# Performance work log

Measured on AMD Instinct MI355X. Metric: run time of the kernel, lower is better.

The kernel has to match this reference:

```python
import jax, jax.numpy as jnp
import numpy as np

NHID = 768
H = 128        # LSTM hidden per direction
NHEADS = 6
NDIR = 12      # 6 heads x 2 directions; first 6 = forward, last 6 = backward
DFF = 4 * NHID
CAT = 2 * H * NHEADS  # 1536


def setup_inputs() -> dict:
    key = jax.random.key(0)
    ks = jax.random.split(key, 12)
    s = 0.05
    return {
        "embeddings": jax.random.normal(ks[0], (16, 512, NHID), jnp.float32),
        # stacked LSTM params; gate order i,f,g,o as in PyTorch
        "W_ih": jax.random.normal(ks[1], (NDIR, 4 * H, NHID), jnp.float32) * s,
        "W_hh": jax.random.normal(ks[2], (NDIR, 4 * H, H), jnp.float32) * s,
        "b_ih": jax.random.normal(ks[3], (NDIR, 4 * H), jnp.float32) * s,
        "b_hh": jax.random.normal(ks[4], (NDIR, 4 * H), jnp.float32) * s,
        "W_int": jax.random.normal(ks[5], (DFF, CAT), jnp.float32) * s,
        "b_int": jax.random.normal(ks[6], (DFF,), jnp.float32) * s,
        "W_out": jax.random.normal(ks[7], (NHID, DFF), jnp.float32) * s,
        "b_out": jax.random.normal(ks[8], (NHID,), jnp.float32) * s,
        "gamma": jnp.ones((NHID,), jnp.float32),
        "beta": jnp.zeros((NHID,), jnp.float32),
    }


def _multi_bilstm(x, W_ih, W_hh, b_ih, b_hh):
    # x: [B,S,D] -> concat of 6 bidirectional LSTM outputs [B,S,1536]
    B, S, _ = x.shape
    # input projections for all 12 directions at once: [12,B,S,4H]
    xp = jnp.einsum('bsd,kgd->kbsg', x, W_ih) + (b_ih + b_hh)[:, None, None, :]
    # reverse time for the 6 backward directions
    xp = jnp.concatenate([xp[:NHEADS], xp[NHEADS:, :, ::-1]], axis=0)
    xs = jnp.moveaxis(xp, 2, 0)  # [S,12,B,4H]

    def step(carry, z_x):
        h, c = carry  # each [12,B,H]
        z = z_x + jnp.einsum('kbh,kgh->kbg', h, W_hh)
        i, f, g, o = jnp.split(z, 4, axis=-1)
        c = jax.nn.sigmoid(f) * c + jax.nn.sigmoid(i) * jnp.tanh(g)
        h = jax.nn.sigmoid(o) * jnp.tanh(c)
        return (h, c), h

    init = (jnp.zeros((NDIR, B, H), x.dtype), jnp.zeros((NDIR, B, H), x.dtype))
    _, ys = jax.lax.scan(step, init, xs)        # [S,12,B,H]
    ys = jnp.moveaxis(ys, 0, 2)                 # [12,B,S,H]
    ys = jnp.concatenate([ys[:NHEADS], ys[NHEADS:, :, ::-1]], axis=0)
    # per-head layout: head0_fwd, head0_bwd, head1_fwd, ... (matches torch.cat of per-LSTM outputs)
    ys = ys.reshape(2, NHEADS, B, S, H).transpose(2, 3, 1, 0, 4)
    return ys.reshape(B, S, CAT)


def reference(embeddings, W_ih, W_hh, b_ih, b_hh, W_int, b_int, W_out, b_out, gamma, beta):
    cat = _multi_bilstm(embeddings, W_ih, W_hh, b_ih, b_hh)
    inter = jax.nn.gelu(cat @ W_int.T + b_int, approximate=False)
    proj = inter @ W_out.T + b_out
    res = embeddings + proj  # dropout is identity (p=0 / eval)
    mu = jnp.mean(res, axis=-1, keepdims=True)
    var = jnp.mean(jnp.square(res - mu), axis=-1, keepdims=True)
    return (res - mu) * jax.lax.rsqrt(var + 1e-5) * gamma + beta
```

## Files before the change

### kernel.cpp

```cpp
#include <hip/hip_runtime.h>

typedef __attribute__((ext_vector_type(4))) float f32x4;
typedef __attribute__((ext_vector_type(8))) short short8;
typedef unsigned short u16;
typedef unsigned int u32;

__device__ __forceinline__ u16 f2bf(float f){
  u32 x = __float_as_uint(f);
  u32 r = x + 0x7fffu + ((x >> 16) & 1u);
  return (u16)(r >> 16);
}
__device__ __forceinline__ float bf2f32(u32 u){ return __uint_as_float(u << 16); }

__device__ __forceinline__ void gld_lds16(const u16* g, u16* l){
  __builtin_amdgcn_global_load_lds((const __attribute__((address_space(1))) void*)g,
                                   (__attribute__((address_space(3))) void*)l, 16, 0, 0);
}

__device__ __forceinline__ f32x4 mfma16(short8 a, short8 b, f32x4 c){
  return __builtin_amdgcn_mfma_f32_16x16x32_bf16(a, b, c, 0, 0, 0);
}

__device__ __forceinline__ float sigf(float x){
  return __builtin_amdgcn_rcpf(1.0f + __expf(-x));
}
__device__ __forceinline__ float tanhf_(float x){
  float e = __expf(2.0f * x);
  return 1.0f - 2.0f * __builtin_amdgcn_rcpf(e + 1.0f);
}

__global__ __launch_bounds__(256) void k_castall(const float* __restrict__ s0, const float* __restrict__ s1,
                          const float* __restrict__ s2, const float* __restrict__ s3,
                          u16* __restrict__ d0, u16* __restrict__ d1, u16* __restrict__ d2,
                          u16* __restrict__ d3)
{
  int i = blockIdx.x * 256 + threadIdx.x;
  const float* s; u16* d; int off;
  if (i < 1572864)      { s = s0; d = d0; off = i; }
  else if (i < 1769472) { s = s1; d = d1; off = i - 1572864; }
  else if (i < 2949120) { s = s2; d = d2; off = i - 1769472; }
  else                  { s = s3; d = d3; off = i - 2949120; }
  float4 v = ((const float4*)s)[off];
  ushort4 o; o.x=f2bf(v.x); o.y=f2bf(v.y); o.z=f2bf(v.z); o.w=f2bf(v.w);
  ((ushort4*)d)[off] = o;
}

__global__ __launch_bounds__(192) void k_permw(const float* __restrict__ wih, u16* __restrict__ dst)
{
  int np = blockIdx.x;
  int d = np >> 9, r = np & 511;
  int src = d*512 + (r & 3)*128 + (r >> 2);
  float4 v = ((const float4*)(wih + (size_t)src*768))[threadIdx.x];
  ushort4 o; o.x=f2bf(v.x); o.y=f2bf(v.y); o.z=f2bf(v.z); o.w=f2bf(v.w);
  ((ushort4*)(dst + (size_t)np*768))[threadIdx.x] = o;
}

template<int MODE, int TPW>
__global__ __launch_bounds__(512) void k_gemmp(
    const u16* __restrict__ A, const u16* __restrict__ B,
    void* __restrict__ C, void* __restrict__ C2,
    const float* __restrict__ bias1, const float* __restrict__ bias2,
    int M, int N, int K, int lda)
{
  __shared__ __align__(16) u16 lA[2][256*64];
  __shared__ __align__(16) u16 lB[3][192*64];
  int nwg = gridDim.x;
  int bid = blockIdx.x;
  int half = 0;
  if (MODE == 2){
    int h2 = nwg >> 1;
    half = (bid >= h2) ? 1 : 0;
    bid -= half ? h2 : 0;
    nwg = h2;
  }
  int koff = half * K;
  int q = nwg >> 3;
  int swz = (bid & 7) * q + (bid >> 3);
  int nbng = N / (192 * TPW);
  int bm = swz / nbng, bng = swz % nbng;
  int tid = threadIdx.x, lane = tid & 63;
  int wv = tid >> 6;
  int wm = wv & 1, wn = wv >> 1;
  int l15 = lane & 15, lhi = lane >> 4;
  const u16* Ag = A + (size_t)(bm << 8) * lda + koff;
  const u16* Bg0 = B + (size_t)(bng * TPW) * 192 * lda + koff;
  size_t bstep = (size_t)192 * lda;

  int srA[4], slA[4];
  #pragma unroll
  for (int i = 0; i < 4; ++i){
    int c = i*512 + tid;
    srA[i] = c >> 3;
    slA[i] = (((c & 7) ^ (srA[i] & 7)) << 3);
  }
  int srB[3], slB[3];
  #pragma unroll
  for (int i = 0; i < 3; ++i){
    int c = i*512 + tid;
    srB[i] = c >> 3;
    slB[i] = (((c & 7) ^ (srB[i] & 7)) << 3);
  }
  int axr = l15 & 7;
  int aoff0 = (wm*128 + l15)*64 + ((lhi    ) ^ axr)*8;
  int aoff1 = (wm*128 + l15)*64 + ((lhi + 4) ^ axr)*8;
  int boff0 = (wn*48  + l15)*64 + ((lhi    ) ^ axr)*8;
  int boff1 = (wn*48  + l15)*64 + ((lhi + 4) ^ axr)*8;

  f32x4 acc[8][3];
  #pragma unroll
  for (int i = 0; i < 8; ++i)
    #pragma unroll
    for (int j = 0; j < 3; ++j)
      acc[i][j] = (f32x4){0.f,0.f,0.f,0.f};

  int NT = K >> 6;
  int TOT = NT * TPW;

#define STAGE_A(SS)                                                            \
  { int ss_ = (SS); int ko = (ss_ % NT) << 6; u16* dA = lA[ss_ & 1];           \
    _Pragma("unroll")                                                          \
    for (int i = 0; i < 4; ++i)                                                \
      gld_lds16(Ag + (size_t)srA[i]*lda + ko + slA[i], &dA[(i*512+tid)*8]); }
#define STAGE_B(SS)                                                            \
  { int ss_ = (SS); int ko = (ss_ % NT) << 6;                                  \
    const u16* Bb = Bg0 + (size_t)(ss_ / NT) * bstep;                          \
    u16* dB = lB[ss_ % 3];                                                     \
    _Pragma("unroll")                                                          \
    for (int i = 0; i < 3; ++i)                                                \
      gld_lds16(Bb + (size_t)srB[i]*lda + ko + slB[i], &dB[(i*512+tid)*8]); }

  STAGE_A(0)
  STAGE_B(0)
  STAGE_B(1)
  asm volatile("s_waitcnt vmcnt(3)" ::: "memory");
  __builtin_amdgcn_s_barrier();

  int kt = 0, tile = 0;
  for (int tt = 0; tt < TOT; ++tt){
    const u16* sA = lA[tt & 1];
    const u16* sB = lB[tt % 3];
    short8 bf[3][2];
    #pragma unroll
    for (int p = 0; p < 4; ++p){
      if (p == 0){
        #pragma unroll
        for (int ni = 0; ni < 3; ++ni){
          bf[ni][0] = *(const short8*)&sB[boff0 + ni*1024];
          bf[ni][1] = *(const short8*)&sB[boff1 + ni*1024];
        }
      }
      short8 a00 = *(const short8*)&sA[aoff0 + (2*p)*1024];
      short8 a01 = *(const short8*)&sA[aoff1 + (2*p)*1024];
      short8 a10 = *(const short8*)&sA[aoff0 + (2*p+1)*1024];
      short8 a11 = *(const short8*)&sA[aoff1 + (2*p+1)*1024];
      if (p == 0 && tt + 1 < TOT){ STAGE_A(tt+1) }
      if (p == 1 && tt + 2 < TOT){ STAGE_B(tt+2) }
      asm volatile("s_barrier" ::: "memory");
      __builtin_amdgcn_s_setprio(1);
      #pragma unroll
      for (int ni = 0; ni < 3; ++ni){
        acc[2*p  ][ni] = mfma16(a00, bf[ni][0], acc[2*p  ][ni]);
        acc[2*p  ][ni] = mfma16(a01, bf[ni][1], acc[2*p  ][ni]);
        acc[2*p+1][ni] = mfma16(a10, bf[ni][0], acc[2*p+1][ni]);
        acc[2*p+1][ni] = mfma16(a11, bf[ni][1], acc[2*p+1][ni]);
      }
      __builtin_amdgcn_s_setprio(0);
      if (p == 3){
        if (tt + 2 < TOT){
          asm volatile("s_waitcnt vmcnt(3)" ::: "memory");
        } else if (tt + 1 < TOT){
          asm volatile("s_waitcnt vmcnt(0)" ::: "memory");
        }
      }
      asm volatile("s_barrier" ::: "memory");
    }

    if (kt == NT - 1){
      int bnbase = (bng * TPW + tile) * 192;
      #pragma unroll
      for (int ni = 0; ni < 3; ++ni){
        int n = bnbase + wn*48 + ni*16 + l15;
        float bs;
        if (MODE == 0){
          int d = n >> 9, r = n & 511;
          int src = d*512 + (r & 3)*128 + (r >> 2);
          bs = bias1[src] + bias2[src];
        } else {
          bs = bias1[n];
        }
        #pragma unroll
        for (int mi = 0; mi < 8; ++mi){
          #pragma unroll
          for (int r = 0; r < 4; ++r){
            int m = (bm << 8) + wm*128 + mi*16 + lhi*4 + r;
            float v = acc[mi][ni][r];
            if (MODE == 2){
              if (!half) v += bs;
              ((float*)(half ? C2 : C))[(size_t)m * N + n] = v;
            } else {
              v += bs;
              if (MODE == 1)
                v = 0.5f * v * (1.0f + erff(v * 0.70710678118f));
              ((u16*)C)[(size_t)m * N + n] = f2bf(v);
            }
            acc[mi][ni][r] = 0.f;
          }
        }
      }
      ++tile; kt = 0;
    } else {
      ++kt;
    }
  }
#undef STAGE_A
#undef STAGE_B
}

__global__ __launch_bounds__(512) void k_scan(const u16* __restrict__ whh, const u16* __restrict__ xp,
                       u16* __restrict__ cat)
{
  __shared__ __align__(16) u16 hb[2][4*144];
  int bid = blockIdx.x;
  int d = bid >> 2, bg = bid & 3;
  int tid = threadIdx.x, lane = tid & 63, w = tid >> 6;
  int l15 = lane & 15, lhi = lane >> 4;

  u16* hbf = (u16*)hb;
  for (int i = tid; i < 2*4*144; i += 512) hbf[i] = 0;

  short8 wf[4][4];
  #pragma unroll
  for (int g = 0; g < 4; ++g)
    #pragma unroll
    for (int kk = 0; kk < 4; ++kk)
      wf[g][kk] = *(const short8*)(whh + ((size_t)d*512 + g*128 + w*16 + l15)*128 + kk*32 + lhi*8);

  int b = bg*4 + lhi;
  int dim = w*16 + l15;
  bool fwd = (d < 6);
  const u16* zbase = xp + (size_t)b*512*6144 + d*512 + dim*4;

  ushort4 Z[4];
  #pragma unroll
  for (int j = 0; j < 4; ++j){
    int s = fwd ? j : 511 - j;
    Z[j] = *(const ushort4*)(zbase + (size_t)s*6144);
  }

  f32x4 a0={0.f,0.f,0.f,0.f}, a1=a0, a2=a0, a3=a0;
  float cr = 0.f;
  int head = fwd ? d : d - 6;
  int posoff = fwd ? 0 : 128;
  size_t catlane = (size_t)b*512*1536 + head*256 + posoff + dim;
  int catoff = fwd ? 0 : 511*1536;
  int catstep = fwd ? 1536 : -1536;

  int hrd = (l15 >> 2)*144 + lhi*8;
  int hwr = lhi*144 + dim;

  __syncthreads();

#define SCAN_STEP(T, RB, WB, S)                                                \
  {                                                                            \
    short8 hf0 = *(const short8*)&hb[RB][hrd + 0*32];                          \
    short8 hf1 = *(const short8*)&hb[RB][hrd + 1*32];                          \
    short8 hf2 = *(const short8*)&hb[RB][hrd + 2*32];                          \
    short8 hf3 = *(const short8*)&hb[RB][hrd + 3*32];                          \
    a0[0] = bf2f32((u32)Z[S].x); a1[0] = bf2f32((u32)Z[S].y);                  \
    a2[0] = bf2f32((u32)Z[S].z); a3[0] = bf2f32((u32)Z[S].w);                  \
    int t4 = (T) + 4; if (t4 > 511) t4 = 511;                                  \
    int s4 = fwd ? t4 : 511 - t4;                                              \
    Z[S] = *(const ushort4*)(zbase + (size_t)s4*6144);                         \
    a2 = mfma16(hf0, wf[2][0], a2); a0 = mfma16(hf0, wf[0][0], a0);            \
    a1 = mfma16(hf0, wf[1][0], a1); a3 = mfma16(hf0, wf[3][0], a3);            \
    a2 = mfma16(hf1, wf[2][1], a2); a0 = mfma16(hf1, wf[0][1], a0);            \
    a1 = mfma16(hf1, wf[1][1], a1); a3 = mfma16(hf1, wf[3][1], a3);            \
    a2 = mfma16(hf2, wf[2][2], a2); a0 = mfma16(hf2, wf[0][2], a0);            \
    a1 = mfma16(hf2, wf[1][2], a1); a3 = mfma16(hf2, wf[3][2], a3);            \
    a2 = mfma16(hf3, wf[2][3], a2); a0 = mfma16(hf3, wf[0][3], a0);            \
    a1 = mfma16(hf3, wf[1][3], a1); a3 = mfma16(hf3, wf[3][3], a3);            \
    float tg = tanhf_(a2[0]);                                                  \
    float fi = sigf(a0[0]), ff = sigf(a1[0]), fo = sigf(a3[0]);                \
    cr = ff*cr + fi*tg;                                                        \
    float hv = fo * tanhf_(cr);                                                \
    u32 hp32;                                                                  \
    asm("v_cvt_pk_bf16_f32 %0, %1, %2" : "=v"(hp32) : "v"(hv), "v"(hv));       \
    u16 hp = (u16)hp32;                                                        \
    hb[WB][hwr] = hp;                                                          \
    cat[catlane + catoff] = hp;                                                \
    catoff += catstep;                                                         \
    asm volatile("s_waitcnt lgkmcnt(0)" ::: "memory");                         \
    __builtin_amdgcn_s_barrier();                                              \
  }

  for (int t = 0; t < 512; t += 4){
    SCAN_STEP(t,   0, 1, 0)
    SCAN_STEP(t+1, 1, 0, 1)
    SCAN_STEP(t+2, 0, 1, 2)
    SCAN_STEP(t+3, 1, 0, 3)
  }
#undef SCAN_STEP
}

__global__ __launch_bounds__(256) void k_ln(const float* __restrict__ emb, const float* __restrict__ p0,
                     const float* __restrict__ p1,
                     const float* __restrict__ gamma, const float* __restrict__ beta,
                     float* __restrict__ out)
{
  int row = blockIdx.x, tid = threadIdx.x;
  const float* pe = emb + (size_t)row * 768;
  const float* pa = p0 + (size_t)row * 768;
  const float* pb = p1 + (size_t)row * 768;
  float v0 = pe[tid]     + pa[tid]     + pb[tid];
  float v1 = pe[tid+256] + pa[tid+256] + pb[tid+256];
  float v2 = pe[tid+512] + pa[tid+512] + pb[tid+512];
  float s = v0+v1+v2, s2 = v0*v0+v1*v1+v2*v2;
  #pragma unroll
  for (int o = 32; o > 0; o >>= 1){ s += __shfl_down(s, o); s2 += __shfl_down(s2, o); }
  __shared__ float rs[4], rq[4];
  int wv = tid >> 6;
  if ((tid & 63) == 0){ rs[wv] = s; rq[wv] = s2; }
  __syncthreads();
  s = rs[0]+rs[1]+rs[2]+rs[3];
  s2 = rq[0]+rq[1]+rq[2]+rq[3];
  float mu = s * (1.0f/768.0f);
  float var = s2 * (1.0f/768.0f) - mu*mu;
  float rr = rsqrtf(var + 1e-5f);
  float* po = out + (size_t)row * 768;
  po[tid]     = (v0-mu)*rr*gamma[tid]     + beta[tid];
  po[tid+256] = (v1-mu)*rr*gamma[tid+256] + beta[tid+256];
  po[tid+512] = (v2-mu)*rr*gamma[tid+512] + beta[tid+512];
}

extern "C" void kernel_launch(void* const* d_in, const int* in_sizes, int n_in,
                              void* d_out, int out_size, void* d_ws, size_t ws_size,
                              hipStream_t stream)
{
  const float* emb   = (const float*)d_in[0];
  const float* W_ih  = (const float*)d_in[1];
  const float* W_hh  = (const float*)d_in[2];
  const float* b_ih  = (const float*)d_in[3];
  const float* b_hh  = (const float*)d_in[4];
  const float* W_int = (const float*)d_in[5];
  const float* b_int = (const float*)d_in[6];
  const float* W_out = (const float*)d_in[7];
  const float* b_out = (const float*)d_in[8];
  const float* gamma = (const float*)d_in[9];
  const float* beta  = (const float*)d_in[10];
  float* out = (float*)d_out;

  char* ws = (char*)d_ws;
  u16* embb  = (u16*)(ws + 0);
  u16* wihb  = (u16*)(ws + 12582912);
  u16* whhb  = (u16*)(ws + 22020096);
  u16* wintb = (u16*)(ws + 23592960);
  u16* woutb = (u16*)(ws + 33030144);
  u16* catb  = (u16*)(ws + 37748736);
  float* proj1=(float*)(ws + 37748736);
  u16* xp    = (u16*)(ws + 62914560);
  u16* interb= (u16*)(ws + 62914560);
  float* proj0=(float*)(ws + 113246208);

  hipLaunchKernelGGL(k_castall, dim3(13824), dim3(256), 0, stream,
                     emb, W_hh, W_int, W_out, embb, whhb, wintb, woutb);
  hipLaunchKernelGGL(k_permw, dim3(6144), dim3(192), 0, stream, W_ih, wihb);

  hipLaunchKernelGGL((k_gemmp<0,4>), dim3(256), dim3(512), 0, stream,
                     embb, wihb, (void*)xp, nullptr, b_ih, b_hh, 8192, 6144, 768, 768);
  hipLaunchKernelGGL(k_scan, dim3(48), dim3(512), 0, stream, whhb, xp, catb);
  hipLaunchKernelGGL((k_gemmp<1,2>), dim3(256), dim3(512), 0, stream,
                     catb, wintb, (void*)interb, nullptr, b_int, nullptr, 8192, 3072, 1536, 1536);
  hipLaunchKernelGGL((k_gemmp<2,1>), dim3(256), dim3(512), 0, stream,
                     interb, woutb, (void*)proj0, (void*)proj1, b_out, nullptr, 8192, 768, 1536, 3072);
  hipLaunchKernelGGL(k_ln, dim3(8192), dim3(256), 0, stream, emb, proj0, proj1, gamma, beta, out);
}
```

Before: 499.3 us.

## Software-pipeline A-fragment LDS reads with MFMAs and drop per-phase barriers

```diff
diff --git a/kernel.cpp b/kernel.cpp
--- a/kernel.cpp
+++ b/kernel.cpp
@@ -129,6 +129,23 @@
     for (int i = 0; i < 3; ++i)                                                \
       gld_lds16(Bb + (size_t)srB[i]*lda + ko + slB[i], &dB[(i*512+tid)*8]); }
 
+#define RD_AF(n0,n1,n2,n3, P)                                                  \
+  n0 = *(const short8*)&sA[aoff0 + (2*(P)  )*1024];                            \
+  n1 = *(const short8*)&sA[aoff1 + (2*(P)  )*1024];                            \
+  n2 = *(const short8*)&sA[aoff0 + (2*(P)+1)*1024];                            \
+  n3 = *(const short8*)&sA[aoff1 + (2*(P)+1)*1024];
+
+#define MFMA_B(P, m0,m1,m2,m3)                                                 \
+  __builtin_amdgcn_s_setprio(1);                                               \
+  _Pragma("unroll")                                                            \
+  for (int ni = 0; ni < 3; ++ni){                                              \
+    acc[2*(P)  ][ni] = mfma16(m0, bf[ni][0], acc[2*(P)  ][ni]);                \
+    acc[2*(P)  ][ni] = mfma16(m1, bf[ni][1], acc[2*(P)  ][ni]);                \
+    acc[2*(P)+1][ni] = mfma16(m2, bf[ni][0], acc[2*(P)+1][ni]);                \
+    acc[2*(P)+1][ni] = mfma16(m3, bf[ni][1], acc[2*(P)+1][ni]);                \
+  }                                                                            \
+  __builtin_amdgcn_s_setprio(0);
+
   STAGE_A(0)
   STAGE_B(0)
   STAGE_B(1)
@@ -141,39 +158,28 @@
     const u16* sB = lB[tt % 3];
     short8 bf[3][2];
     #pragma unroll
-    for (int p = 0; p < 4; ++p){
-      if (p == 0){
-        #pragma unroll
-        for (int ni = 0; ni < 3; ++ni){
-          bf[ni][0] = *(const short8*)&sB[boff0 + ni*1024];
-          bf[ni][1] = *(const short8*)&sB[boff1 + ni*1024];
-        }
-      }
-      short8 a00 = *(const short8*)&sA[aoff0 + (2*p)*1024];
-      short8 a01 = *(const short8*)&sA[aoff1 + (2*p)*1024];
-      short8 a10 = *(const short8*)&sA[aoff0 + (2*p+1)*1024];
-      short8 a11 = *(const short8*)&sA[aoff1 + (2*p+1)*1024];
-      if (p == 0 && tt + 1 < TOT){ STAGE_A(tt+1) }
-      if (p == 1 && tt + 2 < TOT){ STAGE_B(tt+2) }
-      asm volatile("s_barrier" ::: "memory");
-      __builtin_amdgcn_s_setprio(1);
-      #pragma unroll
-      for (int ni = 0; ni < 3; ++ni){
-        acc[2*p  ][ni] = mfma16(a00, bf[ni][0], acc[2*p  ][ni]);
-        acc[2*p  ][ni] = mfma16(a01, bf[ni][1], acc[2*p  ][ni]);
-        acc[2*p+1][ni] = mfma16(a10, bf[ni][0], acc[2*p+1][ni]);
-        acc[2*p+1][ni] = mfma16(a11, bf[ni][1], acc[2*p+1][ni]);
-      }
-      __builtin_amdgcn_s_setprio(0);
-      if (p == 3){
-        if (tt + 2 < TOT){
-          asm volatile("s_waitcnt vmcnt(3)" ::: "memory");
-        } else if (tt + 1 < TOT){
-          asm volatile("s_waitcnt vmcnt(0)" ::: "memory");
-        }
-      }
-      asm volatile("s_barrier" ::: "memory");
+    for (int ni = 0; ni < 3; ++ni){
+      bf[ni][0] = *(const short8*)&sB[boff0 + ni*1024];
+      bf[ni][1] = *(const short8*)&sB[boff1 + ni*1024];
     }
+    short8 x0, x1, x2, x3, y0, y1, y2, y3;
+    RD_AF(x0,x1,x2,x3, 0)
+    if (tt + 1 < TOT){ STAGE_A(tt+1) }
+    if (tt + 2 < TOT){ STAGE_B(tt+2) }
+    RD_AF(y0,y1,y2,y3, 1)
+    MFMA_B(0, x0,x1,x2,x3)
+    RD_AF(x0,x1,x2,x3, 2)
+    MFMA_B(1, y0,y1,y2,y3)
+    RD_AF(y0,y1,y2,y3, 3)
+    MFMA_B(2, x0,x1,x2,x3)
+    MFMA_B(3, y0,y1,y2,y3)
+
+    if (tt + 2 < TOT){
+      asm volatile("s_waitcnt vmcnt(3)" ::: "memory");
+    } else if (tt + 1 < TOT){
+      asm volatile("s_waitcnt vmcnt(0)" ::: "memory");
+    }
+    asm volatile("s_barrier" ::: "memory");
 
     if (kt == NT - 1){
       int bnbase = (bng * TPW + tile) * 192;
@@ -214,6 +220,8 @@
   }
 #undef STAGE_A
 #undef STAGE_B
+#undef RD_AF
+#undef MFMA_B
 }
 
 __global__ __launch_bounds__(512) void k_scan(const u16* __restrict__ whh, const u16* __restrict__ xp,
```

Result: slower. 518.2 us (+3.8%).

## Add 256x256-tile GEMM for input projection and drop mid-tile barrier

Applied to the files above, without the earlier changes.

```diff
diff --git a/kernel.cpp b/kernel.cpp
--- a/kernel.cpp
+++ b/kernel.cpp
@@ -53,6 +53,132 @@
   float4 v = ((const float4*)(wih + (size_t)src*768))[threadIdx.x];
   ushort4 o; o.x=f2bf(v.x); o.y=f2bf(v.y); o.z=f2bf(v.z); o.w=f2bf(v.w);
   ((ushort4*)(dst + (size_t)np*768))[threadIdx.x] = o;
+}
+
+template<int TPW>
+__global__ __launch_bounds__(512) void k_gemmq(
+    const u16* __restrict__ A, const u16* __restrict__ B,
+    u16* __restrict__ C,
+    const float* __restrict__ bias1, const float* __restrict__ bias2,
+    int M, int N, int K, int lda)
+{
+  __shared__ __align__(16) u16 lA[2][256*64];
+  __shared__ __align__(16) u16 lB[2][256*64];
+  int nwg = gridDim.x;
+  int bid = blockIdx.x;
+  int q = nwg >> 3;
+  int swz = (bid & 7) * q + (bid >> 3);
+  int nbng = N / (256 * TPW);
+  int bm = swz / nbng, bng = swz % nbng;
+  int tid = threadIdx.x, lane = tid & 63;
+  int wv = tid >> 6;
+  int wm = wv & 1, wn = wv >> 1;
+  int l15 = lane & 15, lhi = lane >> 4;
+  const u16* Ag = A + (size_t)(bm << 8) * lda;
+  const u16* Bg0 = B + (size_t)(bng * TPW) * 256 * lda;
+  size_t bstep = (size_t)256 * lda;
+
+  int srA[4], slA[4];
+  #pragma unroll
+  for (int i = 0; i < 4; ++i){
+    int c = i*512 + tid;
+    srA[i] = c >> 3;
+    slA[i] = (((c & 7) ^ (srA[i] & 7)) << 3);
+  }
+  int axr = l15 & 7;
+  int aoff0 = (wm*128 + l15)*64 + ((lhi    ) ^ axr)*8;
+  int aoff1 = (wm*128 + l15)*64 + ((lhi + 4) ^ axr)*8;
+  int boff0 = (wn*64  + l15)*64 + ((lhi    ) ^ axr)*8;
+  int boff1 = (wn*64  + l15)*64 + ((lhi + 4) ^ axr)*8;
+
+  f32x4 acc[8][4];
+  #pragma unroll
+  for (int i = 0; i < 8; ++i)
+    #pragma unroll
+    for (int j = 0; j < 4; ++j)
+      acc[i][j] = (f32x4){0.f,0.f,0.f,0.f};
+
+  int NT = K >> 6;
+  int TOT = NT * TPW;
+
+#define STAGE_A(SS)                                                            \
+  { int ss_ = (SS); int ko = (ss_ % NT) << 6; u16* dA = lA[ss_ & 1];           \
+    _Pragma("unroll")                                                          \
+    for (int i = 0; i < 4; ++i)                                                \
+      gld_lds16(Ag + (size_t)srA[i]*lda + ko + slA[i], &dA[(i*512+tid)*8]); }
+#define STAGE_B(SS)                                                            \
+  { int ss_ = (SS); int ko = (ss_ % NT) << 6;                                  \
+    const u16* Bb = Bg0 + (size_t)(ss_ / NT) * bstep;                          \
+    u16* dB = lB[ss_ & 1];                                                     \
+    _Pragma("unroll")                                                          \
+    for (int i = 0; i < 4; ++i)                                                \
+      gld_lds16(Bb + (size_t)srA[i]*lda + ko + slA[i], &dB[(i*512+tid)*8]); }
+
+  STAGE_A(0)
+  STAGE_B(0)
+  asm volatile("s_waitcnt vmcnt(0)" ::: "memory");
+  __builtin_amdgcn_s_barrier();
+
+  int kt = 0, tile = 0;
+  for (int tt = 0; tt < TOT; ++tt){
+    const u16* sA = lA[tt & 1];
+    const u16* sB = lB[tt & 1];
+    short8 bf[4][2];
+    #pragma unroll
+    for (int p = 0; p < 4; ++p){
+      if (p == 0){
+        #pragma unroll
+        for (int ni = 0; ni < 4; ++ni){
+          bf[ni][0] = *(const short8*)&sB[boff0 + ni*1024];
+          bf[ni][1] = *(const short8*)&sB[boff1 + ni*1024];
+        }
+      }
+      short8 a00 = *(const short8*)&sA[aoff0 + (2*p)*1024];
+      short8 a01 = *(const short8*)&sA[aoff1 + (2*p)*1024];
+      short8 a10 = *(const short8*)&sA[aoff0 + (2*p+1)*1024];
+      short8 a11 = *(const short8*)&sA[aoff1 + (2*p+1)*1024];
+      if (p == 0 && tt + 1 < TOT){ STAGE_A(tt+1) }
+      if (p == 1 && tt + 1 < TOT){ STAGE_B(tt+1) }
+      __builtin_amdgcn_s_setprio(1);
+      #pragma unroll
+      for (int ni = 0; ni < 4; ++ni){
+        acc[2*p  ][ni] = mfma16(a00, bf[ni][0], acc[2*p  ][ni]);
+        acc[2*p  ][ni] = mfma16(a01, bf[ni][1], acc[2*p  ][ni]);
+        acc[2*p+1][ni] = mfma16(a10, bf[ni][0], acc[2*p+1][ni]);
+        acc[2*p+1][ni] = mfma16(a11, bf[ni][1], acc[2*p+1][ni]);
+      }
+      __builtin_amdgcn_s_setprio(0);
+      if (p == 3 && tt + 1 < TOT){
+        asm volatile("s_waitcnt vmcnt(0)" ::: "memory");
+      }
+      asm volatile("s_barrier" ::: "memory");
+    }
+
+    if (kt == NT - 1){
+      int bnbase = (bng * TPW + tile) * 256;
+      #pragma unroll
+      for (int ni = 0; ni < 4; ++ni){
+        int n = bnbase + wn*64 + ni*16 + l15;
+        int dd = n >> 9, r9 = n & 511;
+        int src = dd*512 + (r9 & 3)*128 + (r9 >> 2);
+        float bs = bias1[src] + bias2[src];
+        #pragma unroll
+        for (int mi = 0; mi < 8; ++mi){
+          #pragma unroll
+          for (int r = 0; r < 4; ++r){
+            int m = (bm << 8) + wm*128 + mi*16 + lhi*4 + r;
+            C[(size_t)m * N + n] = f2bf(acc[mi][ni][r] + bs);
+            acc[mi][ni][r] = 0.f;
+          }
+        }
+      }
+      ++tile; kt = 0;
+    } else {
+      ++kt;
+    }
+  }
+#undef STAGE_A
+#undef STAGE_B
 }
 
 template<int MODE, int TPW>
@@ -155,7 +281,6 @@
       short8 a11 = *(const short8*)&sA[aoff1 + (2*p+1)*1024];
       if (p == 0 && tt + 1 < TOT){ STAGE_A(tt+1) }
       if (p == 1 && tt + 2 < TOT){ STAGE_B(tt+2) }
-      asm volatile("s_barrier" ::: "memory");
       __builtin_amdgcn_s_setprio(1);
       #pragma unroll
       for (int ni = 0; ni < 3; ++ni){
@@ -365,8 +490,8 @@
                      emb, W_hh, W_int, W_out, embb, whhb, wintb, woutb);
   hipLaunchKernelGGL(k_permw, dim3(6144), dim3(192), 0, stream, W_ih, wihb);
 
-  hipLaunchKernelGGL((k_gemmp<0,4>), dim3(256), dim3(512), 0, stream,
-                     embb, wihb, (void*)xp, nullptr, b_ih, b_hh, 8192, 6144, 768, 768);
+  hipLaunchKernelGGL((k_gemmq<3>), dim3(256), dim3(512), 0, stream,
+                     embb, wihb, xp, b_ih, b_hh, 8192, 6144, 768, 768);
   hipLaunchKernelGGL(k_scan, dim3(48), dim3(512), 0, stream, whhb, xp, catb);
   hipLaunchKernelGGL((k_gemmp<1,2>), dim3(256), dim3(512), 0, stream,
                      catb, wintb, (void*)interb, nullptr, b_int, nullptr, 8192, 3072, 1536, 1536);
```

Result: no change. 495.7 us (-0.7%).
